# Kernel tuning notes

Hardware: AMD Instinct MI355X
Metric: run time of the kernel (lower is better)

Reference implementation:

```python
import jax, jax.numpy as jnp
import numpy as np

B, J, C, K, TOK, CH = 4096, 17, 512, 3, 256, 2048
EPS = 1e-5


def layernorm(x, g, b):
    m = jnp.mean(x, axis=-1, keepdims=True)
    v = jnp.mean(jnp.square(x - m), axis=-1, keepdims=True)
    return (x - m) / jnp.sqrt(v + EPS) * g + b


def gcn(x_bcj, W, b, adj):
    # 1x1 conv to K*C channels: (b,c,v) x (k,o,c) -> (b,k,o,v), then adjacency mix over v
    y = jnp.einsum('bcv,koc->bkov', x_bcj, W) + b[None, :, :, None]
    return jnp.einsum('bkov,kvw->bow', y, adj)  # (b, C, J)


def mlp(x, W1, b1, W2, b2):
    # torch Linear: y = x @ W.T + b ; GELU is exact (erf) in torch default
    h = jax.nn.gelu(x @ W1.T + b1, approximate=False)
    return h @ W2.T + b2


def setup_inputs() -> dict:
    key = jax.random.key(0)
    ks = jax.random.split(key, 8)
    s = lambda fan: 1.0 / np.sqrt(fan)
    return {
        'x': jax.random.normal(ks[0], (B, J, C), jnp.float32),
        'adj': jax.random.uniform(ks[1], (K, J, J), jnp.float32),
        'g1': jnp.ones((J,), jnp.float32), 'be1': jnp.zeros((J,), jnp.float32),
        'g2': jnp.ones((C,), jnp.float32), 'be2': jnp.zeros((C,), jnp.float32),
        'Wg1': jax.random.normal(ks[2], (K, C, C), jnp.float32) * s(C),
        'bg1': jnp.zeros((K, C), jnp.float32),
        'Wg2': jax.random.normal(ks[3], (K, C, C), jnp.float32) * s(C),
        'bg2': jnp.zeros((K, C), jnp.float32),
        'W11': jax.random.normal(ks[4], (TOK, J), jnp.float32) * s(J),
        'b11': jnp.zeros((TOK,), jnp.float32),
        'W12': jax.random.normal(ks[5], (J, TOK), jnp.float32) * s(TOK),
        'b12': jnp.zeros((J,), jnp.float32),
        'W21': jax.random.normal(ks[6], (CH, C), jnp.float32) * s(C),
        'b21': jnp.zeros((CH,), jnp.float32),
        'W22': jax.random.normal(ks[7], (C, CH), jnp.float32) * s(CH),
        'b22': jnp.zeros((C,), jnp.float32),
    }


def reference(x, adj, g1, be1, g2, be2, Wg1, bg1, Wg2, bg2,
              W11, b11, W12, b12, W21, b21, W22, b22):
    # model_type == 'graph_mlp'
    xt = jnp.transpose(x, (0, 2, 1))          # (B, C, J)
    res = xt
    xn = layernorm(xt, g1, be1)               # LN over J (length)
    g1_out = gcn(xn, Wg1, bg1, adj)           # (B, C, J)
    xt = res + mlp(xn, W11, b11, W12, b12) + g1_out
    x2 = jnp.transpose(xt, (0, 2, 1))         # (B, J, C)
    res = x2
    xn = layernorm(x2, g2, be2)               # LN over C (dim)
    g2_out = gcn(jnp.transpose(xn, (0, 2, 1)), Wg2, bg2, adj)  # (B, C, J)
    out = res + mlp(xn, W21, b21, W22, b22) + jnp.transpose(g2_out, (0, 2, 1))
    return out
```

## Files before the change

kernel.cpp:

```cpp
#include <hip/hip_runtime.h>
#include <hip/hip_bf16.h>

#define Bn   4096
#define Jn   17
#define Cn   512
#define Kn   3
#define TOKn 256
#define CHn  2048
#define EPSf 1e-5f
#define Mrows (Bn * Jn)

typedef unsigned short u16;
typedef short bf8_t __attribute__((ext_vector_type(8)));
typedef float f32x4 __attribute__((ext_vector_type(4)));

__device__ __forceinline__ float gelu_fast(float x) {
    float x2 = x * x;
    float z = x * __builtin_fmaf(0.1029474f, x2, 2.3022652f);
    float e = __builtin_amdgcn_exp2f(z);
    float r = __builtin_amdgcn_rcpf(e + 1.0f);
    return x * (1.0f - r);
}
__device__ __forceinline__ float bf2f(u16 u) {
    union { float f; unsigned int i; } w; w.i = ((unsigned int)u) << 16; return w.f;
}
__device__ __forceinline__ u16 f2bf(float f) {
    __hip_bfloat16 h = __float2bfloat16(f);
    union { __hip_bfloat16 h1; u16 u; } cv; cv.h1 = h; return cv.u;
}
__device__ __forceinline__ unsigned pk2(float a, float b) {
    float2 t; t.x = a; t.y = b;
    __hip_bfloat162 h = __float22bfloat162_rn(t);
    union { __hip_bfloat162 h2; unsigned u; } cv; cv.h2 = h; return cv.u;
}
__device__ __forceinline__ void unpack2(unsigned u, float& a, float& b) {
    union { float f; unsigned int i; } t;
    t.i = u << 16;          a = t.f;
    t.i = u & 0xffff0000u;  b = t.f;
}
__device__ __forceinline__ void gload_lds16(const void* g, void* l) {
    __builtin_amdgcn_global_load_lds(
        (const __attribute__((address_space(1))) void*)g,
        (__attribute__((address_space(3))) void*)l, 16, 0, 0);
}

__global__ __launch_bounds__(256) void prep_kernel(
    const float* __restrict__ W21, const float* __restrict__ W22,
    const float* __restrict__ Wg1, const float* __restrict__ Wg2,
    const float* __restrict__ bg1, const float* __restrict__ bg2,
    const float* __restrict__ adj,
    const float* __restrict__ W11, const float* __restrict__ W12,
    u16* __restrict__ W21b, u16* __restrict__ W22b,
    u16* __restrict__ Wg1t, u16* __restrict__ Wg2t,
    float* __restrict__ bias2a, float* __restrict__ bias2b,
    u16* __restrict__ W11p, u16* __restrict__ W12p)
{
    int bid = blockIdx.x, tid = threadIdx.x;
    if (bid < 1024) {
        const float* src = (bid < 512) ? W21 : W22;
        u16* dst = (bid < 512) ? W21b : W22b;
        size_t base = (size_t)(bid & 511) * 2048 + (size_t)tid * 8;
        float4 v0 = *(const float4*)(src + base);
        float4 v1 = *(const float4*)(src + base + 4);
        uint4 o;
        o.x = pk2(v0.x, v0.y); o.y = pk2(v0.z, v0.w);
        o.z = pk2(v1.x, v1.y); o.w = pk2(v1.z, v1.w);
        *(uint4*)(dst + base) = o;
    } else if (bid < 2048) {
        const float* src = (bid < 1536) ? Wg1 : Wg2;
        u16* dst = (bid < 1536) ? Wg1t : Wg2t;
        int rbase = ((bid - 1024) & 511) * 3;
        int c = tid * 2;
        for (int rr = 0; rr < 3; ++rr) {
            int ro = rbase + rr;
            int k = ro >> 9, o = ro & 511;
            const float* sp = src + ((size_t)k * Cn + o) * Cn + c;
            float2 v = *(const float2*)sp;
            *(unsigned*)(dst + (size_t)o * (Kn * Cn) + k * Cn + c) = pk2(v.x, v.y);
        }
    } else if (bid == 2048) {
        __shared__ float adjcs[Kn][Jn];
        for (int i = tid; i < Kn * Jn; i += 256) {
            int k = i / Jn, w = i - k * Jn;
            float s = 0.f;
            for (int v = 0; v < Jn; ++v) s += adj[k * (Jn * Jn) + v * Jn + w];
            adjcs[k][w] = s;
        }
        __syncthreads();
        for (int i = tid; i < Jn * Cn; i += 256) {
            int w = i >> 9, o = i & 511;
            float sa = 0.f, sb = 0.f;
            #pragma unroll
            for (int k = 0; k < Kn; ++k) {
                sa += bg1[k * Cn + o] * adjcs[k][w];
                sb += bg2[k * Cn + o] * adjcs[k][w];
            }
            bias2a[i] = sa; bias2b[i] = sb;
        }
    } else {
        for (int idx = tid; idx < TOKn * 32; idx += 256) {
            int t = idx >> 5, k = idx & 31;
            W11p[idx] = (k < Jn) ? f2bf(W11[t * Jn + k]) : (u16)0;
        }
        for (int idx = tid; idx < 32 * TOKn; idx += 256) {
            int j = idx >> 8, t = idx & 255;
            W12p[idx] = (j < Jn) ? f2bf(W12[j * TOKn + t]) : (u16)0;
        }
    }
}

template<int STAGE>
__global__ __launch_bounds__(256) void premix_kernel(
    const float* __restrict__ x,
    const u16* __restrict__ xn2,
    const float* __restrict__ adj,
    const float* __restrict__ g1, const float* __restrict__ be1,
    float* __restrict__ mean1, float* __restrict__ rstd1,
    u16* __restrict__ xmix)
{
    __shared__ float xsh[Jn][Cn];
    __shared__ float coef[Kn][Jn][Jn];
    __shared__ float s0sh[Kn][Jn];
    __shared__ float s1sh[Kn][Jn];
    __shared__ float msh[Cn], rsh[Cn];
    int b = blockIdx.x, tid = threadIdx.x;

    for (int i = tid; i < Kn * Jn * Jn; i += 256) {
        int k = i / (Jn * Jn); int rem = i - k * (Jn * Jn);
        int v = rem / Jn; int w = rem - v * Jn;
        float av = adj[i];
        coef[k][w][v] = (STAGE == 1) ? av * g1[v] : av;
    }
    if (STAGE == 1) {
        const float* xp = x + (size_t)b * (Jn * Cn);
        for (int i = tid; i < (Jn * Cn) / 4; i += 256)
            ((float4*)&xsh[0][0])[i] = ((const float4*)xp)[i];
    } else {
        const u16* xp = xn2 + (size_t)b * (Jn * Cn);
        for (int i = tid; i < (Jn * Cn) / 8; i += 256) {
            uint4 u = ((const uint4*)xp)[i];
            float* d = &(&xsh[0][0])[i * 8];
            unpack2(u.x, d[0], d[1]); unpack2(u.y, d[2], d[3]);
            unpack2(u.z, d[4], d[5]); unpack2(u.w, d[6], d[7]);
        }
    }
    __syncthreads();
    if (STAGE == 1) {
        for (int c = tid; c < Cn; c += 256) {
            float s = 0.f, q = 0.f;
            #pragma unroll
            for (int v = 0; v < Jn; ++v) { float t = xsh[v][c]; s += t; q += t * t; }
            float m = s * (1.0f / Jn);
            float var = fmaxf(q * (1.0f / Jn) - m * m, 0.f);
            float r = rsqrtf(var + EPSf);
            msh[c] = m; rsh[c] = r;
            mean1[(size_t)b * Cn + c] = m;
            rstd1[(size_t)b * Cn + c] = r;
        }
    }
    if (tid < Kn * Jn) {
        int k = tid / Jn, w = tid - k * Jn;
        float s0 = 0.f, s1 = 0.f;
        #pragma unroll
        for (int v = 0; v < Jn; ++v) {
            if (STAGE == 1) s0 += adj[k * (Jn * Jn) + v * Jn + w] * be1[v];
            s1 += coef[k][w][v];
        }
        s0sh[k][w] = s0; s1sh[k][w] = s1;
    }
    __syncthreads();
    u16* orow = xmix + (size_t)b * Jn * (Kn * Cn);
    for (int k = 0; k < Kn; ++k)
        for (int w = 0; w < Jn; ++w) {
            float cf[Jn];
            #pragma unroll
            for (int v = 0; v < Jn; ++v) cf[v] = coef[k][w][v];
            float ss1 = s1sh[k][w], ss0 = s0sh[k][w];
            for (int c = tid; c < Cn; c += 256) {
                float dot = 0.f;
                #pragma unroll
                for (int v = 0; v < Jn; ++v) dot += cf[v] * xsh[v][c];
                float val;
                if (STAGE == 1) val = rsh[c] * (dot - msh[c] * ss1) + ss0;
                else            val = dot;
                orow[(size_t)w * (Kn * Cn) + k * Cn + c] = f2bf(val);
            }
        }
}

__global__ __launch_bounds__(256) void mlp1_mfma(
    const float* __restrict__ x,
    const float* __restrict__ mean1, const float* __restrict__ rstd1,
    const float* __restrict__ g1, const float* __restrict__ be1,
    const u16* __restrict__ W11p,
    const float* __restrict__ b11,
    const u16* __restrict__ W12p,
    const float* __restrict__ b12,
    float* __restrict__ out)
{
    __shared__ __align__(16) u16 As[128 * 32];
    __shared__ __align__(16) u16 Hs[128 * 128];
    __shared__ __align__(16) u16 W11s[TOKn * 32];
    __shared__ __align__(16) u16 W12s[32 * TOKn];
    __shared__ __align__(16) float b11s[TOKn];
    __shared__ __align__(16) float msrs[256];
    __shared__ float g1s[32], be1s[32];

    int tid = threadIdx.x;
    int lane = tid & 63, wave = tid >> 6;
    int b = blockIdx.y, c0 = blockIdx.x * 128;
    const float* xb = x + (size_t)b * (Jn * Cn);

    #pragma unroll
    for (int t = 0; t < 4; ++t) {
        int idx = t * 256 + tid;
        int tt = idx >> 2, s = idx & 3;
        gload_lds16(W11p + tt * 32 + ((s ^ (tt & 3)) << 3), (char*)W11s + idx * 16);
    }
    #pragma unroll
    for (int t = 0; t < 4; ++t) {
        int idx = t * 256 + tid;
        int j = idx >> 5, s = idx & 31;
        gload_lds16(W12p + j * TOKn + ((s ^ (j & 7)) << 3), (char*)W12s + idx * 16);
    }
    if (wave == 0) gload_lds16(b11 + lane * 4, (char*)b11s + lane * 16);
    if (wave == 1) {
        const float* src = (lane < 32) ? (mean1 + (size_t)b * Cn + c0 + lane * 4)
                                       : (rstd1 + (size_t)b * Cn + c0 + (lane - 32) * 4);
        gload_lds16(src, (char*)msrs + lane * 16);
    }
    if (tid < Jn) { g1s[tid] = g1[tid]; be1s[tid] = be1[tid]; }
    asm volatile("s_waitcnt vmcnt(0)" ::: "memory");
    __syncthreads();

    const float* ms = msrs;
    const float* rs = msrs + 128;
    #pragma unroll
    for (int it = 0; it < 8; ++it) {
        int idx = it * 256 + tid;
        int r = idx & 127, k = (idx >> 7) << 1;
        float mr = ms[r], rr = rs[r];
        float v0 = 0.f, v1 = 0.f;
        if (k < Jn)     v0 = (xb[(size_t)k * Cn + c0 + r] - mr) * rr * g1s[k] + be1s[k];
        if (k + 1 < Jn) v1 = (xb[(size_t)(k + 1) * Cn + c0 + r] - mr) * rr * g1s[k + 1] + be1s[k + 1];
        *(unsigned*)((char*)As + r * 64 + ((((k >> 3) ^ (r & 3))) << 4) + ((k & 7) << 1)) = pk2(v0, v1);
    }
    __syncthreads();

    int rb = wave * 32;
    f32x4 acc2[2][2];
    #pragma unroll
    for (int i = 0; i < 2; ++i)
        #pragma unroll
        for (int j = 0; j < 2; ++j) acc2[i][j] = (f32x4)0.f;

    bf8_t bfc[2];
    #pragma unroll
    for (int cf = 0; cf < 2; ++cf) {
        int c = rb + cf * 16 + (lane & 15);
        bfc[cf] = *(const bf8_t*)((const char*)As + c * 64 + ((((lane >> 4)) ^ (c & 3)) << 4));
    }

    #pragma unroll
    for (int ch = 0; ch < 2; ++ch) {
        f32x4 acc1[8][2];
        #pragma unroll
        for (int tf = 0; tf < 8; ++tf)
            #pragma unroll
            for (int cf = 0; cf < 2; ++cf) acc1[tf][cf] = (f32x4)0.f;
        #pragma unroll
        for (int tf = 0; tf < 8; ++tf) {
            int t = ch * 128 + tf * 16 + (lane & 15);
            bf8_t aw = *(const bf8_t*)((const char*)W11s + t * 64 + ((((lane >> 4)) ^ (t & 3)) << 4));
            #pragma unroll
            for (int cf = 0; cf < 2; ++cf)
                acc1[tf][cf] = __builtin_amdgcn_mfma_f32_16x16x32_bf16(aw, bfc[cf], acc1[tf][cf], 0, 0, 0);
        }
        #pragma unroll
        for (int tf = 0; tf < 8; ++tf) {
            int t0 = tf * 16 + ((lane >> 4) << 2);
            float bq0 = b11s[ch * 128 + t0 + 0];
            float bq1 = b11s[ch * 128 + t0 + 1];
            float bq2 = b11s[ch * 128 + t0 + 2];
            float bq3 = b11s[ch * 128 + t0 + 3];
            #pragma unroll
            for (int cf = 0; cf < 2; ++cf) {
                int c = rb + cf * 16 + (lane & 15);
                float h0 = gelu_fast(acc1[tf][cf][0] + bq0);
                float h1 = gelu_fast(acc1[tf][cf][1] + bq1);
                float h2 = gelu_fast(acc1[tf][cf][2] + bq2);
                float h3 = gelu_fast(acc1[tf][cf][3] + bq3);
                uint2 w; w.x = pk2(h0, h1); w.y = pk2(h2, h3);
                *(uint2*)((char*)Hs + c * 256 + ((((t0 >> 3) ^ (c & 7))) << 4) + ((t0 & 7) << 1)) = w;
            }
        }
        #pragma unroll
        for (int kt = 0; kt < 4; ++kt) {
            bf8_t bh[2];
            #pragma unroll
            for (int cf = 0; cf < 2; ++cf) {
                int c = rb + cf * 16 + (lane & 15);
                int tc = kt * 4 + (lane >> 4);
                bh[cf] = *(const bf8_t*)((const char*)Hs + c * 256 + ((tc ^ (c & 7)) << 4));
            }
            #pragma unroll
            for (int jf = 0; jf < 2; ++jf) {
                int j = jf * 16 + (lane & 15);
                int tc = ch * 16 + kt * 4 + (lane >> 4);
                bf8_t aw = *(const bf8_t*)((const char*)W12s + j * 512 + ((tc ^ (j & 7)) << 4));
                #pragma unroll
                for (int cf = 0; cf < 2; ++cf)
                    acc2[jf][cf] = __builtin_amdgcn_mfma_f32_16x16x32_bf16(aw, bh[cf], acc2[jf][cf], 0, 0, 0);
            }
        }
    }

    #pragma unroll
    for (int jf = 0; jf < 2; ++jf) {
        #pragma unroll
        for (int cf = 0; cf < 2; ++cf) {
            int c = c0 + rb + cf * 16 + (lane & 15);
            #pragma unroll
            for (int i = 0; i < 4; ++i) {
                int j = jf * 16 + ((lane >> 4) << 2) + i;
                if (j < Jn) {
                    size_t off = (size_t)b * (Jn * Cn) + (size_t)j * Cn + c;
                    out[off] = x[off] + acc2[jf][cf][i] + b12[j];
                }
            }
        }
    }
}

__global__ __launch_bounds__(256) void ln2_kernel(const float* __restrict__ X2,
        const float* __restrict__ g2, const float* __restrict__ be2,
        u16* __restrict__ xn2)
{
    int row = blockIdx.x * 4 + (threadIdx.x >> 6);
    int lane = threadIdx.x & 63;
    const float* p = X2 + (size_t)row * Cn;
    float4 v0 = ((const float4*)p)[lane];
    float4 v1 = ((const float4*)p)[lane + 64];
    float s = v0.x + v0.y + v0.z + v0.w + v1.x + v1.y + v1.z + v1.w;
    float q = v0.x*v0.x + v0.y*v0.y + v0.z*v0.z + v0.w*v0.w
            + v1.x*v1.x + v1.y*v1.y + v1.z*v1.z + v1.w*v1.w;
    #pragma unroll
    for (int off = 32; off > 0; off >>= 1) { s += __shfl_xor(s, off); q += __shfl_xor(q, off); }
    float mean = s * (1.0f / Cn);
    float var = fmaxf(q * (1.0f / Cn) - mean * mean, 0.f);
    float rs = rsqrtf(var + EPSf);
    float4 ga = ((const float4*)g2)[lane],      ba = ((const float4*)be2)[lane];
    float4 gb = ((const float4*)g2)[lane + 64], bb = ((const float4*)be2)[lane + 64];
    uint2 w0, w1;
    w0.x = pk2((v0.x-mean)*rs*ga.x + ba.x, (v0.y-mean)*rs*ga.y + ba.y);
    w0.y = pk2((v0.z-mean)*rs*ga.z + ba.z, (v0.w-mean)*rs*ga.w + ba.w);
    w1.x = pk2((v1.x-mean)*rs*gb.x + bb.x, (v1.y-mean)*rs*gb.y + bb.y);
    w1.y = pk2((v1.z-mean)*rs*gb.z + bb.z, (v1.w-mean)*rs*gb.w + bb.w);
    ((uint2*)(xn2 + (size_t)row * Cn))[lane] = w0;
    ((uint2*)(xn2 + (size_t)row * Cn))[lane + 64] = w1;
}

template<int EPI>
__global__ __launch_bounds__(256) void gemm_bt(
    const u16* __restrict__ A, int ldA,
    const u16* __restrict__ Bt, int ldB,
    int K, int Nld,
    const float* __restrict__ bias,
    float* __restrict__ outF, u16* __restrict__ outH)
{
    __shared__ __align__(16) u16 As[2][128 * 32];
    __shared__ __align__(16) u16 Bs[2][128 * 32];
    int tid = threadIdx.x;
    int gx = gridDim.x;
    int total = gx * gridDim.y;
    int lid = blockIdx.y * gx + blockIdx.x;
    int cpx = total >> 3;
    int wg = (lid & 7) * cpx + (lid >> 3);
    int n0 = (wg % gx) << 7;
    int m0 = (wg / gx) << 7;

    int wave = tid >> 6, lane = tid & 63;
    int wr = wave >> 1, wc = wave & 1;

    const u16* aSrc[2]; const u16* bSrc[2];
    #pragma unroll
    for (int t = 0; t < 2; ++t) {
        int idx = t * 256 + tid;
        int r = idx >> 2;
        int cs = (idx & 3) ^ ((r >> 1) & 3);
        aSrc[t] = A  + (size_t)(m0 + r) * ldA + cs * 8;
        bSrc[t] = Bt + (size_t)(n0 + r) * ldB + cs * 8;
    }
    int aOff[4], bOff[4];
    #pragma unroll
    for (int i = 0; i < 4; ++i) {
        int ra = wr * 64 + i * 16 + (lane & 15);
        aOff[i] = ra * 64 + ((((lane >> 4)) ^ ((ra >> 1) & 3)) << 4);
        int rb = wc * 64 + i * 16 + (lane & 15);
        bOff[i] = rb * 64 + ((((lane >> 4)) ^ ((rb >> 1) & 3)) << 4);
    }

    f32x4 acc[4][4];
    #pragma unroll
    for (int i = 0; i < 4; ++i)
        #pragma unroll
        for (int j = 0; j < 4; ++j) acc[i][j] = (f32x4)0.f;

    int KT = K >> 5;
    #pragma unroll
    for (int t = 0; t < 2; ++t) {
        int idx = t * 256 + tid;
        gload_lds16(aSrc[t], (char*)&As[0][0] + idx * 16);
        gload_lds16(bSrc[t], (char*)&Bs[0][0] + idx * 16);
    }
    int cur = 0;
    for (int kt = 0; kt < KT; ++kt) {
        asm volatile("s_waitcnt vmcnt(0)" ::: "memory");
        __syncthreads();
        if (kt + 1 < KT) {
            int k0 = (kt + 1) << 5;
            #pragma unroll
            for (int t = 0; t < 2; ++t) {
                int idx = t * 256 + tid;
                gload_lds16(aSrc[t] + k0, (char*)&As[cur ^ 1][0] + idx * 16);
                gload_lds16(bSrc[t] + k0, (char*)&Bs[cur ^ 1][0] + idx * 16);
            }
        }
        bf8_t af[4], bfr[4];
        #pragma unroll
        for (int i = 0; i < 4; ++i) {
            af[i]  = *(const bf8_t*)((const char*)&As[cur][0] + aOff[i]);
            bfr[i] = *(const bf8_t*)((const char*)&Bs[cur][0] + bOff[i]);
        }
        #pragma unroll
        for (int mi = 0; mi < 4; ++mi)
            #pragma unroll
            for (int ni = 0; ni < 4; ++ni)
                acc[mi][ni] = __builtin_amdgcn_mfma_f32_16x16x32_bf16(af[mi], bfr[ni], acc[mi][ni], 0, 0, 0);
        cur ^= 1;
    }

    #pragma unroll
    for (int mi = 0; mi < 4; ++mi) {
        int rbase = m0 + wr * 64 + mi * 16 + ((lane >> 4) << 2);
        #pragma unroll
        for (int ni = 0; ni < 4; ++ni) {
            int col = n0 + wc * 64 + ni * 16 + (lane & 15);
            if (EPI == 0) {
                float bv = bias[col];
                #pragma unroll
                for (int i = 0; i < 4; ++i) {
                    float v = gelu_fast(acc[mi][ni][i] + bv);
                    outH[(size_t)(rbase + i) * Nld + col] = f2bf(v);
                }
            } else if (EPI == 1) {
                float bv = bias ? bias[col] : 0.f;
                #pragma unroll
                for (int i = 0; i < 4; ++i) {
                    size_t off = (size_t)(rbase + i) * Nld + col;
                    outF[off] += acc[mi][ni][i] + bv;
                }
            } else {
                #pragma unroll
                for (int i = 0; i < 4; ++i) {
                    int row = rbase + i;
                    int w = row % Jn;
                    size_t off = (size_t)row * Nld + col;
                    outF[off] += acc[mi][ni][i] + bias[w * Cn + col];
                }
            }
        }
    }
}

extern "C" void kernel_launch(void* const* d_in, const int* in_sizes, int n_in,
                              void* d_out, int out_size, void* d_ws, size_t ws_size,
                              hipStream_t stream)
{
    (void)in_sizes; (void)n_in; (void)out_size; (void)ws_size;
    const float* x   = (const float*)d_in[0];
    const float* adj = (const float*)d_in[1];
    const float* g1  = (const float*)d_in[2];
    const float* be1 = (const float*)d_in[3];
    const float* g2  = (const float*)d_in[4];
    const float* be2 = (const float*)d_in[5];
    const float* Wg1 = (const float*)d_in[6];
    const float* bg1 = (const float*)d_in[7];
    const float* Wg2 = (const float*)d_in[8];
    const float* bg2 = (const float*)d_in[9];
    const float* W11 = (const float*)d_in[10];
    const float* b11 = (const float*)d_in[11];
    const float* W12 = (const float*)d_in[12];
    const float* b12 = (const float*)d_in[13];
    const float* W21 = (const float*)d_in[14];
    const float* b21 = (const float*)d_in[15];
    const float* W22 = (const float*)d_in[16];
    const float* b22 = (const float*)d_in[17];
    float* out = (float*)d_out;

    char* p = (char*)d_ws;
    float* mean1  = (float*)p;                 p += (size_t)Bn * Cn * 4;
    float* rstd1  = (float*)p;                 p += (size_t)Bn * Cn * 4;
    u16*   xn2    = (u16*)p;                   p += (size_t)Mrows * Cn * 2;
    u16*   W21b   = (u16*)p;                   p += (size_t)CHn * Cn * 2;
    u16*   W22b   = (u16*)p;                   p += (size_t)CHn * Cn * 2;
    u16*   Wg1t   = (u16*)p;                   p += (size_t)Cn * Kn * Cn * 2;
    u16*   Wg2t   = (u16*)p;                   p += (size_t)Cn * Kn * Cn * 2;
    float* bias2a = (float*)p;                 p += (size_t)Jn * Cn * 4;
    float* bias2b = (float*)p;                 p += (size_t)Jn * Cn * 4;
    u16*   W11p   = (u16*)p;                   p += (size_t)TOKn * 32 * 2;
    u16*   W12p   = (u16*)p;                   p += (size_t)32 * TOKn * 2;
    u16*   xmix   = (u16*)p;
    u16*   Hbuf   = xmix;

    prep_kernel<<<2050, 256, 0, stream>>>(W21, W22, Wg1, Wg2, bg1, bg2, adj, W11, W12,
                                          W21b, W22b, Wg1t, Wg2t, bias2a, bias2b, W11p, W12p);
    premix_kernel<1><<<Bn, 256, 0, stream>>>(x, (const u16*)nullptr, adj, g1, be1, mean1, rstd1, xmix);
    {
        dim3 g(Cn / 128, Bn);
        mlp1_mfma<<<g, 256, 0, stream>>>(x, mean1, rstd1, g1, be1, W11p, b11, W12p, b12, out);
    }
    {
        dim3 g(Cn / 128, Mrows / 128);
        gemm_bt<2><<<g, 256, 0, stream>>>(xmix, Kn * Cn, Wg1t, Kn * Cn, Kn * Cn, Cn, bias2a, out, (u16*)nullptr);
    }
    ln2_kernel<<<Mrows / 4, 256, 0, stream>>>(out, g2, be2, xn2);
    for (int h = 0; h < 2; ++h) {
        int hc = h * 1024;
        dim3 ga(1024 / 128, Mrows / 128);
        gemm_bt<0><<<ga, 256, 0, stream>>>(xn2, Cn, W21b + (size_t)hc * Cn, Cn, Cn, 1024, b21 + hc, (float*)nullptr, Hbuf);
        dim3 gb(Cn / 128, Mrows / 128);
        gemm_bt<1><<<gb, 256, 0, stream>>>(Hbuf, 1024, W22b + hc, CHn, 1024, Cn, (h == 0) ? b22 : (const float*)nullptr, out, (u16*)nullptr);
    }
    premix_kernel<2><<<Bn, 256, 0, stream>>>((const float*)nullptr, xn2, adj, (const float*)nullptr, (const float*)nullptr,
                                             (float*)nullptr, (float*)nullptr, xmix);
    {
        dim3 g(Cn / 128, Mrows / 128);
        gemm_bt<2><<<g, 256, 0, stream>>>(xmix, Kn * Cn, Wg2t, Kn * Cn, Kn * Cn, Cn, bias2b, out, (u16*)nullptr);
    }
}
```

Measured before the change: 1.880 ms.

## Repack W11 and A tiles to cut LDS conflicts, vectorize premix, unsplit MLP2

Three unrelated changes. W11 is stored as k-chunk-major planes and the As tile gets a padded 80-byte row stride with a different XOR swizzle, both meant to reduce LDS bank conflicts in the first MLP's MFMA fragment loads. The premix kernel now has each thread handle two adjacent channels and write packed bf16 pairs, and hoists the per-channel mean and rstd out of the k,w loop. When the workspace is large enough, the second MLP runs as one full-width hidden GEMM pair instead of two halves, at the cost of a larger hidden buffer and more memory traffic for it.

Measured after the change: 1.631 ms. 13.2% less time.

```diff
diff --git a/kernel.cpp b/kernel.cpp
--- a/kernel.cpp
+++ b/kernel.cpp
@@ -98,9 +98,10 @@
             bias2a[i] = sa; bias2b[i] = sb;
         }
     } else {
-        for (int idx = tid; idx < TOKn * 32; idx += 256) {
-            int t = idx >> 5, k = idx & 31;
-            W11p[idx] = (k < Jn) ? f2bf(W11[t * Jn + k]) : (u16)0;
+        for (int i = tid; i < 4 * TOKn * 8; i += 256) {
+            int ck = i >> 11, t = (i >> 3) & 255, e = i & 7;
+            int k = ck * 8 + e;
+            W11p[i] = (k < Jn) ? f2bf(W11[t * Jn + k]) : (u16)0;
         }
         for (int idx = tid; idx < 32 * TOKn; idx += 256) {
             int j = idx >> 8, t = idx & 255;
@@ -170,21 +171,24 @@
     }
     __syncthreads();
     u16* orow = xmix + (size_t)b * Jn * (Kn * Cn);
+    int c = tid * 2;
+    float m0v = 0.f, m1v = 0.f, r0v = 1.f, r1v = 1.f;
+    if (STAGE == 1) { m0v = msh[c]; m1v = msh[c + 1]; r0v = rsh[c]; r1v = rsh[c + 1]; }
     for (int k = 0; k < Kn; ++k)
         for (int w = 0; w < Jn; ++w) {
             float cf[Jn];
             #pragma unroll
             for (int v = 0; v < Jn; ++v) cf[v] = coef[k][w][v];
-            float ss1 = s1sh[k][w], ss0 = s0sh[k][w];
-            for (int c = tid; c < Cn; c += 256) {
-                float dot = 0.f;
-                #pragma unroll
-                for (int v = 0; v < Jn; ++v) dot += cf[v] * xsh[v][c];
-                float val;
-                if (STAGE == 1) val = rsh[c] * (dot - msh[c] * ss1) + ss0;
-                else            val = dot;
-                orow[(size_t)w * (Kn * Cn) + k * Cn + c] = f2bf(val);
-            }
+            float d0 = 0.f, d1 = 0.f;
+            #pragma unroll
+            for (int v = 0; v < Jn; ++v) { d0 += cf[v] * xsh[v][c]; d1 += cf[v] * xsh[v][c + 1]; }
+            float v0, v1;
+            if (STAGE == 1) {
+                float ss1 = s1sh[k][w], ss0 = s0sh[k][w];
+                v0 = r0v * (d0 - m0v * ss1) + ss0;
+                v1 = r1v * (d1 - m1v * ss1) + ss0;
+            } else { v0 = d0; v1 = d1; }
+            *(unsigned*)(orow + (size_t)w * (Kn * Cn) + k * Cn + c) = pk2(v0, v1);
         }
 }
 
@@ -198,9 +202,9 @@
     const float* __restrict__ b12,
     float* __restrict__ out)
 {
-    __shared__ __align__(16) u16 As[128 * 32];
+    __shared__ __align__(16) u16 As[128 * 40];
     __shared__ __align__(16) u16 Hs[128 * 128];
-    __shared__ __align__(16) u16 W11s[TOKn * 32];
+    __shared__ __align__(16) u16 W11s[4 * TOKn * 8];
     __shared__ __align__(16) u16 W12s[32 * TOKn];
     __shared__ __align__(16) float b11s[TOKn];
     __shared__ __align__(16) float msrs[256];
@@ -214,8 +218,7 @@
     #pragma unroll
     for (int t = 0; t < 4; ++t) {
         int idx = t * 256 + tid;
-        int tt = idx >> 2, s = idx & 3;
-        gload_lds16(W11p + tt * 32 + ((s ^ (tt & 3)) << 3), (char*)W11s + idx * 16);
+        gload_lds16(W11p + idx * 8, (char*)W11s + idx * 16);
     }
     #pragma unroll
     for (int t = 0; t < 4; ++t) {
@@ -243,7 +246,8 @@
         float v0 = 0.f, v1 = 0.f;
         if (k < Jn)     v0 = (xb[(size_t)k * Cn + c0 + r] - mr) * rr * g1s[k] + be1s[k];
         if (k + 1 < Jn) v1 = (xb[(size_t)(k + 1) * Cn + c0 + r] - mr) * rr * g1s[k + 1] + be1s[k + 1];
-        *(unsigned*)((char*)As + r * 64 + ((((k >> 3) ^ (r & 3))) << 4) + ((k & 7) << 1)) = pk2(v0, v1);
+        int ck = (k >> 3) ^ ((r >> 3) & 3);
+        *(unsigned*)((char*)As + r * 80 + (ck << 4) + ((k & 7) << 1)) = pk2(v0, v1);
     }
     __syncthreads();
 
@@ -258,7 +262,8 @@
     #pragma unroll
     for (int cf = 0; cf < 2; ++cf) {
         int c = rb + cf * 16 + (lane & 15);
-        bfc[cf] = *(const bf8_t*)((const char*)As + c * 64 + ((((lane >> 4)) ^ (c & 3)) << 4));
+        int ck = (lane >> 4) ^ ((c >> 3) & 3);
+        bfc[cf] = *(const bf8_t*)((const char*)As + c * 80 + (ck << 4));
     }
 
     #pragma unroll
@@ -271,7 +276,7 @@
         #pragma unroll
         for (int tf = 0; tf < 8; ++tf) {
             int t = ch * 128 + tf * 16 + (lane & 15);
-            bf8_t aw = *(const bf8_t*)((const char*)W11s + t * 64 + ((((lane >> 4)) ^ (t & 3)) << 4));
+            bf8_t aw = *(const bf8_t*)((const char*)W11s + ((lane >> 4) << 12) + t * 16);
             #pragma unroll
             for (int cf = 0; cf < 2; ++cf)
                 acc1[tf][cf] = __builtin_amdgcn_mfma_f32_16x16x32_bf16(aw, bfc[cf], acc1[tf][cf], 0, 0, 0);
@@ -477,7 +482,7 @@
                               void* d_out, int out_size, void* d_ws, size_t ws_size,
                               hipStream_t stream)
 {
-    (void)in_sizes; (void)n_in; (void)out_size; (void)ws_size;
+    (void)in_sizes; (void)n_in; (void)out_size;
     const float* x   = (const float*)d_in[0];
     const float* adj = (const float*)d_in[1];
     const float* g1  = (const float*)d_in[2];
@@ -508,10 +513,13 @@
     u16*   Wg2t   = (u16*)p;                   p += (size_t)Cn * Kn * Cn * 2;
     float* bias2a = (float*)p;                 p += (size_t)Jn * Cn * 4;
     float* bias2b = (float*)p;                 p += (size_t)Jn * Cn * 4;
-    u16*   W11p   = (u16*)p;                   p += (size_t)TOKn * 32 * 2;
+    u16*   W11p   = (u16*)p;                   p += (size_t)4 * TOKn * 8 * 2;
     u16*   W12p   = (u16*)p;                   p += (size_t)32 * TOKn * 2;
     u16*   xmix   = (u16*)p;
     u16*   Hbuf   = xmix;
+
+    size_t fixedBytes = (size_t)((char*)xmix - (char*)d_ws);
+    bool fullH = ws_size >= fixedBytes + (size_t)Mrows * CHn * 2;
 
     prep_kernel<<<2050, 256, 0, stream>>>(W21, W22, Wg1, Wg2, bg1, bg2, adj, W11, W12,
                                           W21b, W22b, Wg1t, Wg2t, bias2a, bias2b, W11p, W12p);
@@ -525,12 +533,19 @@
         gemm_bt<2><<<g, 256, 0, stream>>>(xmix, Kn * Cn, Wg1t, Kn * Cn, Kn * Cn, Cn, bias2a, out, (u16*)nullptr);
     }
     ln2_kernel<<<Mrows / 4, 256, 0, stream>>>(out, g2, be2, xn2);
-    for (int h = 0; h < 2; ++h) {
-        int hc = h * 1024;
-        dim3 ga(1024 / 128, Mrows / 128);
-        gemm_bt<0><<<ga, 256, 0, stream>>>(xn2, Cn, W21b + (size_t)hc * Cn, Cn, Cn, 1024, b21 + hc, (float*)nullptr, Hbuf);
+    if (fullH) {
+        dim3 ga(CHn / 128, Mrows / 128);
+        gemm_bt<0><<<ga, 256, 0, stream>>>(xn2, Cn, W21b, Cn, Cn, CHn, b21, (float*)nullptr, Hbuf);
         dim3 gb(Cn / 128, Mrows / 128);
-        gemm_bt<1><<<gb, 256, 0, stream>>>(Hbuf, 1024, W22b + hc, CHn, 1024, Cn, (h == 0) ? b22 : (const float*)nullptr, out, (u16*)nullptr);
+        gemm_bt<1><<<gb, 256, 0, stream>>>(Hbuf, CHn, W22b, CHn, CHn, Cn, b22, out, (u16*)nullptr);
+    } else {
+        for (int h = 0; h < 2; ++h) {
+            int hc = h * 1024;
+            dim3 ga(1024 / 128, Mrows / 128);
+            gemm_bt<0><<<ga, 256, 0, stream>>>(xn2, Cn, W21b + (size_t)hc * Cn, Cn, Cn, 1024, b21 + hc, (float*)nullptr, Hbuf);
+            dim3 gb(Cn / 128, Mrows / 128);
+            gemm_bt<1><<<gb, 256, 0, stream>>>(Hbuf, 1024, W22b + hc, CHn, 1024, Cn, (h == 0) ? b22 : (const float*)nullptr, out, (u16*)nullptr);
+        }
     }
     premix_kernel<2><<<Bn, 256, 0, stream>>>((const float*)nullptr, xn2, adj, (const float*)nullptr, (const float*)nullptr,
                                              (float*)nullptr, (float*)nullptr, xmix);
```
